# Kernel optimization log

Hardware: AMD Instinct MI355X
Metric: run time of the kernel (lower is better)

## Reference

```python
import jax, jax.numpy as jnp
import numpy as np

B, V, S, E, K, FF = 16, 512, 1024, 8, 2, 2048  # batch, n_vars, seq_len, n_experts, top_k, ff_dim


def setup_inputs() -> dict:
    key = jax.random.key(0)
    ks = jax.random.split(key, 6)
    def w(k, shape, fan_in):
        return (jax.random.normal(k, shape, jnp.float32) / np.sqrt(fan_in)).astype(jnp.float32)
    return {
        "x": jax.random.normal(ks[0], (B, S, V), jnp.float32),
        "gate_W": w(ks[1], (E, S), S),          # Gating: Linear(seq_len -> n_experts), no bias
        "exp_W": w(ks[2], (E, S, S), S),        # per-expert Linear(seq_len -> seq_len) weights
        "exp_b": jnp.zeros((E, S), jnp.float32),
        "fc1_W": w(ks[3], (FF, V), V),          # MLPFeat fc1: Linear(n_vars -> ff_dim)
        "fc1_b": jnp.zeros((FF,), jnp.float32),
        "fc2_W": w(ks[4], (V, FF), FF),         # MLPFeat fc2: Linear(ff_dim -> n_vars)
        "fc2_b": jnp.zeros((V,), jnp.float32),
    }


def reference(x, gate_W, exp_W, exp_b, fc1_W, fc1_b, fc2_W, fc2_b):
    # Dropout layers are identity at inference.
    res = x                                   # [B,S,V]
    xt = jnp.swapaxes(x, 1, 2)                # [B,V,S] tokens of dim seq_len

    # --- MLPTime (multi_expert MoE) ---
    logits = jnp.einsum('bvs,es->bve', xt, gate_W)      # [B,V,E]
    probs = jax.nn.softmax(logits, axis=-1)             # gate_logits returned by torch code
    w, sel = jax.lax.top_k(probs, K)                    # [B,V,K]
    # combine top-k weights into a dense per-expert weight [B,V,E] (zeros off top-k)
    full_w = jnp.sum(jax.nn.one_hot(sel, E, dtype=xt.dtype) * w[..., None], axis=2)
    # all-expert outputs, then weighted combine (same math as the per-expert scatter loop)
    all_out = jnp.einsum('bvs,eos->bveo', xt, exp_W) + exp_b[None, None]  # [B,V,E,S]
    moe = jnp.einsum('bve,bveo->bvo', full_w, all_out)                    # [B,V,S]
    t = jax.nn.relu(moe)

    x = jnp.swapaxes(t, 1, 2) + res           # [B,S,V] residual

    # --- MLPFeat ---
    res2 = x
    h = jax.nn.relu(x @ fc1_W.T + fc1_b)      # [B,S,FF]
    x = h @ fc2_W.T + fc2_b + res2            # [B,S,V]
    return (x, probs)
```

## Files before the change

### kernel.cpp

```cpp
#include <hip/hip_runtime.h>
#include <stdint.h>

#define B_  16
#define V_  512
#define S_  1024
#define E_  8
#define FF_ 2048
#define NT_ (B_*V_)
#define NR_ (B_*S_)

typedef __attribute__((ext_vector_type(8))) short bf16x8;
typedef __attribute__((ext_vector_type(4))) float f32x4;

__device__ __forceinline__ unsigned short f2bf(float f) {
    unsigned int u = __float_as_uint(f);
    u += 0x7FFFu + ((u >> 16) & 1u);
    return (unsigned short)(u >> 16);
}
__device__ __forceinline__ float bf2f(unsigned short u) {
    return __uint_as_float(((unsigned int)u) << 16);
}

__device__ __forceinline__ void gl_lds16(const void* g, void* l) {
    __builtin_amdgcn_global_load_lds((const __attribute__((address_space(1))) void*)g,
                                     (__attribute__((address_space(3))) void*)l,
                                     16, 0, 0);
}

__device__ __forceinline__ void cvt4(const float* s, unsigned short* d, int i) {
    float4 v = *(const float4*)(s + i);
    ushort4 o; o.x = f2bf(v.x); o.y = f2bf(v.y); o.z = f2bf(v.z); o.w = f2bf(v.w);
    *(ushort4*)(d + i) = o;
}
__global__ void k_convert3(const float* __restrict__ s0, unsigned short* __restrict__ d0, int g0,
                           const float* __restrict__ s1, unsigned short* __restrict__ d1, int g1,
                           const float* __restrict__ s2, unsigned short* __restrict__ d2) {
    int g = blockIdx.x * 256 + threadIdx.x;
    if (g < g0)           cvt4(s0, d0, g * 4);
    else if (g < g0 + g1) cvt4(s1, d1, (g - g0) * 4);
    else                  cvt4(s2, d2, (g - g0 - g1) * 4);
}

__global__ __launch_bounds__(256) void k_xt_gate(const float* __restrict__ x,
                                                 const float* __restrict__ gate_W,
                                                 unsigned short* __restrict__ xt,
                                                 double* __restrict__ part,
                                                 int* __restrict__ cnt) {
    __shared__ float t[32][33];
    __shared__ float gw[E_][128];
    int b = blockIdx.z, sc = blockIdx.y, vt = blockIdx.x;
    int tid = threadIdx.x;
    if (vt == 0 && sc == 0 && b == 0 && tid < E_) cnt[tid] = 0;
    int col = tid & 31, row8 = tid >> 5;
    for (int i = tid; i < E_ * 128; i += 256) {
        int e = i >> 7, j = i & 127;
        gw[e][j] = gate_W[e * S_ + sc * 128 + j];
    }
    double acc = 0.0;
    for (int sub = 0; sub < 4; ++sub) {
        int s0 = sc * 128 + sub * 32;
        __syncthreads();
        for (int r = 0; r < 4; ++r) {
            int sl = row8 + r * 8;
            t[sl][col] = x[(b * S_ + s0 + sl) * V_ + vt * 32 + col];
        }
        __syncthreads();
        for (int r = 0; r < 4; ++r) {
            int vl = row8 + r * 8;
            xt[(size_t)(b * V_ + vt * 32 + vl) * S_ + s0 + col] = f2bf(t[col][vl]);
        }
        #pragma unroll
        for (int s = 0; s < 32; ++s)
            acc += (double)t[s][col] * (double)gw[row8][sub * 32 + s];
    }
    int tok = b * V_ + vt * 32 + col;
    part[((size_t)sc * NT_ + tok) * E_ + row8] = acc;
}

__global__ __launch_bounds__(256) void k_gate_fin(const double* __restrict__ part,
                                                  float* __restrict__ probs_out,
                                                  int* __restrict__ cnt, int* __restrict__ tok_of,
                                                  int* __restrict__ tk_slot, float* __restrict__ tk_w) {
    int t = blockIdx.x * 256 + threadIdx.x;
    int lane = threadIdx.x & 63;
    double l[E_];
    #pragma unroll
    for (int e = 0; e < E_; ++e) l[e] = 0.0;
    for (int c = 0; c < S_ / 128; ++c) {
        const double* p = part + ((size_t)c * NT_ + t) * E_;
        #pragma unroll
        for (int e = 0; e < E_; ++e) l[e] += p[e];
    }
    double m = l[0];
    #pragma unroll
    for (int e = 1; e < E_; ++e) m = l[e] > m ? l[e] : m;
    double p[E_], sum = 0.0;
    #pragma unroll
    for (int e = 0; e < E_; ++e) { p[e] = exp(l[e] - m); sum += p[e]; }
    float pf[E_];
    #pragma unroll
    for (int e = 0; e < E_; ++e) pf[e] = (float)(p[e] / sum);
    float4 pa = {pf[0], pf[1], pf[2], pf[3]}, pb = {pf[4], pf[5], pf[6], pf[7]};
    *(float4*)(probs_out + (size_t)t * E_) = pa;
    *(float4*)(probs_out + (size_t)t * E_ + 4) = pb;
    int i0 = 0;
    #pragma unroll
    for (int e = 1; e < E_; ++e) if (pf[e] > pf[i0]) i0 = e;
    int i1 = -1;
    #pragma unroll
    for (int e = 0; e < E_; ++e) if (e != i0 && (i1 < 0 || pf[e] > pf[i1])) i1 = e;
    int sel[2] = {i0, i1};
    float wsel[2] = {pf[i0], pf[i1]};
    #pragma unroll
    for (int k = 0; k < 2; ++k) {
        int ie = sel[k];
        int pos = 0;
        for (int e = 0; e < E_; ++e) {
            unsigned long long msk = __ballot(ie == e);
            if (ie == e) {
                int rank = __popcll(msk & ((1ull << lane) - 1ull));
                int leader = __ffsll((long long)msk) - 1;
                int base = 0;
                if (lane == leader) base = atomicAdd(&cnt[e], __popcll(msk));
                base = __shfl(base, leader);
                pos = base + rank;
            }
        }
        tok_of[ie * NT_ + pos] = t;
        tk_slot[t * 2 + k] = (ie << 16) | pos;
        tk_w[t * 2 + k] = wsel[k];
    }
}

__device__ __forceinline__ void gemm_k_loop64(const unsigned short* (&ap)[4],
                                              const unsigned short* (&bp)[4],
                                              short* As, short* Bs, int kIters, int wave, int lane,
                                              f32x4 (&acc)[4][4]) {
    char* ldsA = (char*)As + wave * 4096;
    char* ldsB = (char*)Bs + wave * 4096;
    int wm = (wave & 1) << 6, wn = (wave >> 1) << 6;
    int lr = lane & 15, quad = lane >> 4;
    int pb = (quad ^ (lr & 7)) * 8;
    const unsigned short* a0 = ap[0]; const unsigned short* a1 = ap[1];
    const unsigned short* a2 = ap[2]; const unsigned short* a3 = ap[3];
    const unsigned short* b0 = bp[0]; const unsigned short* b1 = bp[1];
    const unsigned short* b2 = bp[2]; const unsigned short* b3 = bp[3];
    for (int kk = 0; kk < kIters; ++kk) {
        gl_lds16(a0, ldsA);        gl_lds16(a1, ldsA + 1024);
        gl_lds16(a2, ldsA + 2048); gl_lds16(a3, ldsA + 3072);
        gl_lds16(b0, ldsB);        gl_lds16(b1, ldsB + 1024);
        gl_lds16(b2, ldsB + 2048); gl_lds16(b3, ldsB + 3072);
        a0 += 64; a1 += 64; a2 += 64; a3 += 64;
        b0 += 64; b1 += 64; b2 += 64; b3 += 64;
        __syncthreads();
        #pragma unroll
        for (int ks = 0; ks < 2; ++ks) {
            int po = pb ^ (ks << 5);
            bf16x8 af[4], bfv[4];
            #pragma unroll
            for (int i = 0; i < 4; ++i)
                af[i] = *(const bf16x8*)(As + (wm + i * 16 + lr) * 64 + po);
            #pragma unroll
            for (int j = 0; j < 4; ++j)
                bfv[j] = *(const bf16x8*)(Bs + (wn + j * 16 + lr) * 64 + po);
            #pragma unroll
            for (int i = 0; i < 4; ++i)
                #pragma unroll
                for (int j = 0; j < 4; ++j)
                    acc[i][j] = __builtin_amdgcn_mfma_f32_16x16x32_bf16(af[i], bfv[j], acc[i][j], 0, 0, 0);
        }
        __syncthreads();
    }
}

__global__ __launch_bounds__(256, 3) void k_moe_gemm(const unsigned short* __restrict__ xt,
                                                     const unsigned short* __restrict__ expWb,
                                                     const float* __restrict__ exp_b,
                                                     const int* __restrict__ cnt,
                                                     const int* __restrict__ tok_of,
                                                     unsigned short* __restrict__ Yb) {
    int bx = ((int)(blockIdx.x & 7)) * 17 + (int)(blockIdx.x >> 3);
    int e = -1, pos0 = 0, yrow0 = 0, ne = 0;
    {
        int tb = 0, o = 0;
        #pragma unroll
        for (int i = 0; i < E_; ++i) {
            int ci = cnt[i];
            int nti = (ci + 127) >> 7;
            if (e < 0 && bx < tb + nti) { e = i; pos0 = (bx - tb) * 128; yrow0 = o; ne = ci; }
            tb += nti; o += ci;
        }
    }
    if (e < 0) return;
    int nt = blockIdx.y;
    __shared__ __align__(16) short As[128 * 64];
    __shared__ __align__(16) short Bs[128 * 64];
    int tid = threadIdx.x, wave = tid >> 6, lane = tid & 63;
    int rowLoc = wave * 32 + (lane >> 3);
    int cg = ((lane & 7) ^ ((lane >> 3) & 7)) * 8;
    const unsigned short* Wb = expWb + (size_t)e * S_ * S_;
    const unsigned short* ap[4];
    const unsigned short* bp[4];
    #pragma unroll
    for (int c = 0; c < 4; ++c) {
        int rr = rowLoc + c * 8;
        int tok = tok_of[e * NT_ + min(pos0 + rr, ne - 1)];
        ap[c] = xt + (size_t)tok * S_ + cg;
        bp[c] = Wb + (size_t)(nt * 128 + rr) * S_ + cg;
    }
    f32x4 acc[4][4] = {};
    gemm_k_loop64(ap, bp, As, Bs, S_ / 64, wave, lane, acc);
    int wm = (wave & 1) << 6, wn = (wave >> 1) << 6;
    int lr = lane & 15, quad = lane >> 4;
    #pragma unroll
    for (int i = 0; i < 4; ++i)
        #pragma unroll
        for (int r = 0; r < 4; ++r) {
            int pos = pos0 + wm + i * 16 + quad * 4 + r;
            if (pos < ne) {
                size_t row = (size_t)(yrow0 + pos);
                #pragma unroll
                for (int j = 0; j < 4; ++j) {
                    int col = nt * 128 + wn + j * 16 + lr;
                    Yb[row * S_ + col] = f2bf(acc[i][j][r] + exp_b[e * S_ + col]);
                }
            }
        }
}

__global__ void k_combine(const float* __restrict__ x, const unsigned short* __restrict__ Yb,
                          const int* __restrict__ cnt, const int* __restrict__ tk_slot,
                          const float* __restrict__ tk_w,
                          unsigned short* __restrict__ x2b) {
    __shared__ float t[32][33];
    int b = blockIdx.z, st = blockIdx.y, vt = blockIdx.x;
    int tid = threadIdx.x;
    int vl = tid >> 3, sq = (tid & 7) * 4;
    int tok = b * V_ + vt * 32 + vl;
    int s0 = tk_slot[tok * 2 + 0], s1 = tk_slot[tok * 2 + 1];
    float w0 = tk_w[tok * 2 + 0], w1 = tk_w[tok * 2 + 1];
    int e0 = s0 >> 16, e1 = s1 >> 16;
    int r0b = 0, r1b = 0, o = 0;
    #pragma unroll
    for (int i = 0; i < E_; ++i) {
        if (i == e0) r0b = o;
        if (i == e1) r1b = o;
        o += cnt[i];
    }
    size_t r0 = (size_t)(r0b + (s0 & 0xFFFF));
    size_t r1 = (size_t)(r1b + (s1 & 0xFFFF));
    int sg = st * 32 + sq;
    ushort4 y0 = *(const ushort4*)(Yb + r0 * S_ + sg);
    ushort4 y1 = *(const ushort4*)(Yb + r1 * S_ + sg);
    t[vl][sq + 0] = fmaxf(w0 * bf2f(y0.x) + w1 * bf2f(y1.x), 0.f);
    t[vl][sq + 1] = fmaxf(w0 * bf2f(y0.y) + w1 * bf2f(y1.y), 0.f);
    t[vl][sq + 2] = fmaxf(w0 * bf2f(y0.z) + w1 * bf2f(y1.z), 0.f);
    t[vl][sq + 3] = fmaxf(w0 * bf2f(y0.w) + w1 * bf2f(y1.w), 0.f);
    __syncthreads();
    int vcol = tid & 31, srow8 = tid >> 5;
    for (int r = 0; r < 4; ++r) {
        int sl = srow8 + r * 8;
        size_t gi = (size_t)(b * S_ + st * 32 + sl) * V_ + vt * 32 + vcol;
        x2b[gi] = f2bf(x[gi] + t[vcol][sl]);
    }
}

__global__ __launch_bounds__(256, 3) void k_fc1(const unsigned short* __restrict__ x2b,
                                                const unsigned short* __restrict__ w1b,
                                                const float* __restrict__ fc1_b,
                                                unsigned short* __restrict__ h) {
    __shared__ __align__(16) short As[128 * 64];
    __shared__ __align__(16) short Bs[128 * 64];
    int tid = threadIdx.x, wave = tid >> 6, lane = tid & 63;
    int rowLoc = wave * 32 + (lane >> 3);
    int cg = ((lane & 7) ^ ((lane >> 3) & 7)) * 8;
    int m0 = blockIdx.x * 128, n0 = blockIdx.y * 128;
    const unsigned short* ap[4];
    const unsigned short* bp[4];
    #pragma unroll
    for (int c = 0; c < 4; ++c) {
        int rr = rowLoc + c * 8;
        ap[c] = x2b + (size_t)(m0 + rr) * V_ + cg;
        bp[c] = w1b + (size_t)(n0 + rr) * V_ + cg;
    }
    f32x4 acc[4][4] = {};
    gemm_k_loop64(ap, bp, As, Bs, V_ / 64, wave, lane, acc);
    int wm = (wave & 1) << 6, wn = (wave >> 1) << 6;
    int lr = lane & 15, quad = lane >> 4;
    #pragma unroll
    for (int i = 0; i < 4; ++i)
        #pragma unroll
        for (int r = 0; r < 4; ++r) {
            size_t row = (size_t)(m0 + wm + i * 16 + quad * 4 + r);
            #pragma unroll
            for (int j = 0; j < 4; ++j) {
                int col = n0 + wn + j * 16 + lr;
                h[row * FF_ + col] = f2bf(fmaxf(acc[i][j][r] + fc1_b[col], 0.f));
            }
        }
}

__global__ __launch_bounds__(256, 3) void k_fc2(const unsigned short* __restrict__ h,
                                                const unsigned short* __restrict__ w2b,
                                                const float* __restrict__ fc2_b,
                                                const unsigned short* __restrict__ x2b,
                                                float* __restrict__ out) {
    __shared__ __align__(16) short As[128 * 64];
    __shared__ __align__(16) short Bs[128 * 64];
    int tid = threadIdx.x, wave = tid >> 6, lane = tid & 63;
    int rowLoc = wave * 32 + (lane >> 3);
    int cg = ((lane & 7) ^ ((lane >> 3) & 7)) * 8;
    int m0 = blockIdx.x * 128, n0 = blockIdx.y * 128;
    const unsigned short* ap[4];
    const unsigned short* bp[4];
    #pragma unroll
    for (int c = 0; c < 4; ++c) {
        int rr = rowLoc + c * 8;
        ap[c] = h + (size_t)(m0 + rr) * FF_ + cg;
        bp[c] = w2b + (size_t)(n0 + rr) * FF_ + cg;
    }
    f32x4 acc[4][4] = {};
    gemm_k_loop64(ap, bp, As, Bs, FF_ / 64, wave, lane, acc);
    int wm = (wave & 1) << 6, wn = (wave >> 1) << 6;
    int lr = lane & 15, quad = lane >> 4;
    #pragma unroll
    for (int i = 0; i < 4; ++i)
        #pragma unroll
        for (int r = 0; r < 4; ++r) {
            size_t row = (size_t)(m0 + wm + i * 16 + quad * 4 + r);
            #pragma unroll
            for (int j = 0; j < 4; ++j) {
                int col = n0 + wn + j * 16 + lr;
                out[row * V_ + col] = acc[i][j][r] + fc2_b[col] + bf2f(x2b[row * V_ + col]);
            }
        }
}

extern "C" void kernel_launch(void* const* d_in, const int* in_sizes, int n_in,
                              void* d_out, int out_size, void* d_ws, size_t ws_size,
                              hipStream_t stream) {
    const float* x      = (const float*)d_in[0];
    const float* gate_W = (const float*)d_in[1];
    const float* exp_W  = (const float*)d_in[2];
    const float* exp_b  = (const float*)d_in[3];
    const float* fc1_W  = (const float*)d_in[4];
    const float* fc1_b  = (const float*)d_in[5];
    const float* fc2_W  = (const float*)d_in[6];
    const float* fc2_b  = (const float*)d_in[7];
    float* out_x = (float*)d_out;
    float* out_p = (float*)d_out + (size_t)B_ * S_ * V_;

    if (ws_size < (size_t)155582592) return;

    char* ws = (char*)d_ws;
    unsigned short* Yb    = (unsigned short*)(ws);
    unsigned short* xt    = (unsigned short*)(ws +  67108864);
    unsigned short* x2b   = (unsigned short*)(ws + 117440512);
    unsigned short* expWb = (unsigned short*)(ws + 134217728);
    unsigned short* fc1Wb = (unsigned short*)(ws + 150994944);
    unsigned short* fc2Wb = (unsigned short*)(ws + 153092096);
    char* route = ws + 155189248;
    int*   cnt     = (int*)(route);
    int*   tok_of  = (int*)(route + 128);
    int*   tk_slot = (int*)(route + 128 + 262144);
    float* tk_w    = (float*)(route + 128 + 262144 + 65536);
    unsigned short* h = (unsigned short*)ws;
    double* part = (double*)ws;

    k_convert3<<<dim3((2097152 + 262144 + 262144) / 256), 256, 0, stream>>>(
        exp_W, expWb, 2097152, fc1_W, fc1Wb, 262144, fc2_W, fc2Wb);
    k_xt_gate<<<dim3(V_ / 32, S_ / 128, B_), 256, 0, stream>>>(x, gate_W, xt, part, cnt);
    k_gate_fin<<<dim3(NT_ / 256), 256, 0, stream>>>(part, out_p, cnt, tok_of, tk_slot, tk_w);
    k_moe_gemm<<<dim3(136, S_ / 128), 256, 0, stream>>>(xt, expWb, exp_b, cnt, tok_of, Yb);
    k_combine<<<dim3(V_ / 32, S_ / 32, B_), 256, 0, stream>>>(x, Yb, cnt, tk_slot, tk_w, x2b);
    k_fc1<<<dim3(NR_ / 128, FF_ / 128), 256, 0, stream>>>(x2b, fc1Wb, fc1_b, h);
    k_fc2<<<dim3(NR_ / 128, V_ / 128), 256, 0, stream>>>(h, fc2Wb, fc2_b, x2b, out_x);
}
```

Measured before the change: 305.7 us.

## Use 256x256 double-buffered 8-wave GEMM tiles for MoE and fc1

Replaces the 128x128 single-buffer 4-wave GEMMs for the expert projection and fc1 with a 256x256-tile, 512-thread kernel. It double-buffers LDS (128KB dynamic shared memory), prefetches the next K-slab while the current one computes, and interleaves barriers with MFMA priority hints in the ping-pong style. The aim is more data reuse per tile and overlap of global loads with MFMA work. The cost is one block per CU, larger padding waste for MoE tiles of 256 tokens, and fewer blocks for fc1. It also depends on the dynamic LDS size being accepted by the launch.

Result: slower. 330.8 us (+8.2%).

```diff
diff --git a/kernel.cpp b/kernel.cpp
--- a/kernel.cpp
+++ b/kernel.cpp
@@ -130,6 +130,170 @@
         tk_slot[t * 2 + k] = (ie << 16) | pos;
         tk_w[t * 2 + k] = wsel[k];
     }
+}
+
+__device__ __forceinline__ void stage8(const unsigned short* (&ap)[4],
+                                       const unsigned short* (&bp)[4],
+                                       char* ldsA, char* ldsB, int kt, int wave) {
+    const int off = kt * 64;
+    char* la = ldsA + wave * 4096;
+    char* lb = ldsB + wave * 4096;
+    gl_lds16(ap[0] + off, la);
+    gl_lds16(ap[1] + off, la + 1024);
+    gl_lds16(ap[2] + off, la + 2048);
+    gl_lds16(ap[3] + off, la + 3072);
+    gl_lds16(bp[0] + off, lb);
+    gl_lds16(bp[1] + off, lb + 1024);
+    gl_lds16(bp[2] + off, lb + 2048);
+    gl_lds16(bp[3] + off, lb + 3072);
+}
+
+template<bool LAST>
+__device__ __forceinline__ void body64(const short* As, const short* Bs,
+                                       int wmBase, int wnBase, int lr, int pb,
+                                       f32x4 (&acc)[8][4]) {
+    if (LAST) asm volatile("s_waitcnt vmcnt(0)" ::: "memory");
+    else      asm volatile("s_waitcnt vmcnt(8)" ::: "memory");
+    __builtin_amdgcn_s_barrier();
+    __builtin_amdgcn_sched_barrier(0);
+    bf16x8 bfv[4][2];
+    #pragma unroll
+    for (int j = 0; j < 4; ++j)
+        #pragma unroll
+        for (int ks = 0; ks < 2; ++ks)
+            bfv[j][ks] = *(const bf16x8*)(Bs + (wnBase + j * 16 + lr) * 64 + (pb ^ (ks << 5)));
+    #pragma unroll
+    for (int q = 0; q < 4; ++q) {
+        bf16x8 af[2][2];
+        #pragma unroll
+        for (int f = 0; f < 2; ++f)
+            #pragma unroll
+            for (int ks = 0; ks < 2; ++ks)
+                af[f][ks] = *(const bf16x8*)(As + (wmBase + q * 32 + f * 16 + lr) * 64 + (pb ^ (ks << 5)));
+        __builtin_amdgcn_s_barrier();
+        __builtin_amdgcn_s_setprio(1);
+        #pragma unroll
+        for (int f = 0; f < 2; ++f)
+            #pragma unroll
+            for (int j = 0; j < 4; ++j)
+                #pragma unroll
+                for (int ks = 0; ks < 2; ++ks)
+                    acc[q * 2 + f][j] = __builtin_amdgcn_mfma_f32_16x16x32_bf16(
+                        af[f][ks], bfv[j][ks], acc[q * 2 + f][j], 0, 0, 0);
+        __builtin_amdgcn_s_setprio(0);
+        __builtin_amdgcn_s_barrier();
+    }
+}
+
+template<int KT>
+__device__ __forceinline__ void gemm8(const unsigned short* (&ap)[4],
+                                      const unsigned short* (&bp)[4],
+                                      char* smem, int wave, int lane,
+                                      f32x4 (&acc)[8][4]) {
+    char* A0 = smem;           char* B0 = smem + 32768;
+    char* A1 = smem + 65536;   char* B1 = smem + 98304;
+    const int wmBase = (wave >> 2) * 128;
+    const int wnBase = (wave & 3) * 64;
+    const int lr = lane & 15;
+    const int pb = ((lane >> 4) ^ (lr & 7)) * 8;
+    stage8(ap, bp, A0, B0, 0, wave);
+    stage8(ap, bp, A1, B1, 1, wave);
+    for (int kt = 0; kt + 2 < KT; kt += 2) {
+        body64<false>((const short*)A0, (const short*)B0, wmBase, wnBase, lr, pb, acc);
+        stage8(ap, bp, A0, B0, kt + 2, wave);
+        body64<false>((const short*)A1, (const short*)B1, wmBase, wnBase, lr, pb, acc);
+        stage8(ap, bp, A1, B1, kt + 3, wave);
+    }
+    body64<false>((const short*)A0, (const short*)B0, wmBase, wnBase, lr, pb, acc);
+    body64<true >((const short*)A1, (const short*)B1, wmBase, wnBase, lr, pb, acc);
+}
+
+__global__ __launch_bounds__(512, 1) void k_moe_gemm8(const unsigned short* __restrict__ xt,
+                                                      const unsigned short* __restrict__ expWb,
+                                                      const float* __restrict__ exp_b,
+                                                      const int* __restrict__ cnt,
+                                                      const int* __restrict__ tok_of,
+                                                      unsigned short* __restrict__ Yb) {
+    int bx = ((int)(blockIdx.x & 7)) * 9 + (int)(blockIdx.x >> 3);
+    int e = -1, pos0 = 0, yrow0 = 0, ne = 0;
+    {
+        int tb = 0, o = 0;
+        #pragma unroll
+        for (int i = 0; i < E_; ++i) {
+            int ci = cnt[i];
+            int nti = (ci + 255) >> 8;
+            if (e < 0 && bx < tb + nti) { e = i; pos0 = (bx - tb) * 256; yrow0 = o; ne = ci; }
+            tb += nti; o += ci;
+        }
+    }
+    if (e < 0) return;
+    int nt = blockIdx.y;
+    extern __shared__ char smem[];
+    int tid = threadIdx.x, wave = tid >> 6, lane = tid & 63;
+    int rowLoc = wave * 32 + (lane >> 3);
+    int cg = ((lane & 7) ^ ((lane >> 3) & 7)) * 8;
+    const unsigned short* Wb = expWb + (size_t)e * S_ * S_;
+    const unsigned short* ap[4];
+    const unsigned short* bp[4];
+    #pragma unroll
+    for (int c = 0; c < 4; ++c) {
+        int rr = rowLoc + c * 8;
+        int tok = tok_of[e * NT_ + min(pos0 + rr, ne - 1)];
+        ap[c] = xt + (size_t)tok * S_ + cg;
+        bp[c] = Wb + (size_t)(nt * 256 + rr) * S_ + cg;
+    }
+    f32x4 acc[8][4] = {};
+    gemm8<S_ / 64>(ap, bp, smem, wave, lane, acc);
+    int wmBase = (wave >> 2) * 128, wnBase = (wave & 3) * 64;
+    int lr = lane & 15, quad = lane >> 4;
+    #pragma unroll
+    for (int i = 0; i < 8; ++i)
+        #pragma unroll
+        for (int r = 0; r < 4; ++r) {
+            int pos = pos0 + wmBase + i * 16 + quad * 4 + r;
+            if (pos < ne) {
+                size_t row = (size_t)(yrow0 + pos);
+                #pragma unroll
+                for (int j = 0; j < 4; ++j) {
+                    int col = nt * 256 + wnBase + j * 16 + lr;
+                    Yb[row * S_ + col] = f2bf(acc[i][j][r] + exp_b[e * S_ + col]);
+                }
+            }
+        }
+}
+
+__global__ __launch_bounds__(512, 1) void k_fc1_8p(const unsigned short* __restrict__ x2b,
+                                                   const unsigned short* __restrict__ w1b,
+                                                   const float* __restrict__ fc1_b,
+                                                   unsigned short* __restrict__ h) {
+    extern __shared__ char smem[];
+    int tid = threadIdx.x, wave = tid >> 6, lane = tid & 63;
+    int m0 = blockIdx.x * 256, n0 = blockIdx.y * 256;
+    int rowLoc = wave * 32 + (lane >> 3);
+    int cg = ((lane & 7) ^ ((lane >> 3) & 7)) * 8;
+    const unsigned short* ap[4];
+    const unsigned short* bp[4];
+    #pragma unroll
+    for (int c = 0; c < 4; ++c) {
+        int rr = rowLoc + c * 8;
+        ap[c] = x2b + (size_t)(m0 + rr) * V_ + cg;
+        bp[c] = w1b + (size_t)(n0 + rr) * V_ + cg;
+    }
+    f32x4 acc[8][4] = {};
+    gemm8<V_ / 64>(ap, bp, smem, wave, lane, acc);
+    int wmBase = (wave >> 2) * 128, wnBase = (wave & 3) * 64;
+    int lr = lane & 15, quad = lane >> 4;
+    #pragma unroll
+    for (int i = 0; i < 8; ++i)
+        #pragma unroll
+        for (int r = 0; r < 4; ++r) {
+            size_t row = (size_t)(m0 + wmBase + i * 16 + quad * 4 + r);
+            #pragma unroll
+            for (int j = 0; j < 4; ++j) {
+                int col = n0 + wnBase + j * 16 + lr;
+                h[row * FF_ + col] = f2bf(fmaxf(acc[i][j][r] + fc1_b[col], 0.f));
+            }
+        }
 }
 
 __device__ __forceinline__ void gemm_k_loop64(const unsigned short* (&ap)[4],
@@ -173,61 +337,6 @@
     }
 }
 
-__global__ __launch_bounds__(256, 3) void k_moe_gemm(const unsigned short* __restrict__ xt,
-                                                     const unsigned short* __restrict__ expWb,
-                                                     const float* __restrict__ exp_b,
-                                                     const int* __restrict__ cnt,
-                                                     const int* __restrict__ tok_of,
-                                                     unsigned short* __restrict__ Yb) {
-    int bx = ((int)(blockIdx.x & 7)) * 17 + (int)(blockIdx.x >> 3);
-    int e = -1, pos0 = 0, yrow0 = 0, ne = 0;
-    {
-        int tb = 0, o = 0;
-        #pragma unroll
-        for (int i = 0; i < E_; ++i) {
-            int ci = cnt[i];
-            int nti = (ci + 127) >> 7;
-            if (e < 0 && bx < tb + nti) { e = i; pos0 = (bx - tb) * 128; yrow0 = o; ne = ci; }
-            tb += nti; o += ci;
-        }
-    }
-    if (e < 0) return;
-    int nt = blockIdx.y;
-    __shared__ __align__(16) short As[128 * 64];
-    __shared__ __align__(16) short Bs[128 * 64];
-    int tid = threadIdx.x, wave = tid >> 6, lane = tid & 63;
-    int rowLoc = wave * 32 + (lane >> 3);
-    int cg = ((lane & 7) ^ ((lane >> 3) & 7)) * 8;
-    const unsigned short* Wb = expWb + (size_t)e * S_ * S_;
-    const unsigned short* ap[4];
-    const unsigned short* bp[4];
-    #pragma unroll
-    for (int c = 0; c < 4; ++c) {
-        int rr = rowLoc + c * 8;
-        int tok = tok_of[e * NT_ + min(pos0 + rr, ne - 1)];
-        ap[c] = xt + (size_t)tok * S_ + cg;
-        bp[c] = Wb + (size_t)(nt * 128 + rr) * S_ + cg;
-    }
-    f32x4 acc[4][4] = {};
-    gemm_k_loop64(ap, bp, As, Bs, S_ / 64, wave, lane, acc);
-    int wm = (wave & 1) << 6, wn = (wave >> 1) << 6;
-    int lr = lane & 15, quad = lane >> 4;
-    #pragma unroll
-    for (int i = 0; i < 4; ++i)
-        #pragma unroll
-        for (int r = 0; r < 4; ++r) {
-            int pos = pos0 + wm + i * 16 + quad * 4 + r;
-            if (pos < ne) {
-                size_t row = (size_t)(yrow0 + pos);
-                #pragma unroll
-                for (int j = 0; j < 4; ++j) {
-                    int col = nt * 128 + wn + j * 16 + lr;
-                    Yb[row * S_ + col] = f2bf(acc[i][j][r] + exp_b[e * S_ + col]);
-                }
-            }
-        }
-}
-
 __global__ void k_combine(const float* __restrict__ x, const unsigned short* __restrict__ Yb,
                           const int* __restrict__ cnt, const int* __restrict__ tk_slot,
                           const float* __restrict__ tk_w,
@@ -265,41 +374,6 @@
     }
 }
 
-__global__ __launch_bounds__(256, 3) void k_fc1(const unsigned short* __restrict__ x2b,
-                                                const unsigned short* __restrict__ w1b,
-                                                const float* __restrict__ fc1_b,
-                                                unsigned short* __restrict__ h) {
-    __shared__ __align__(16) short As[128 * 64];
-    __shared__ __align__(16) short Bs[128 * 64];
-    int tid = threadIdx.x, wave = tid >> 6, lane = tid & 63;
-    int rowLoc = wave * 32 + (lane >> 3);
-    int cg = ((lane & 7) ^ ((lane >> 3) & 7)) * 8;
-    int m0 = blockIdx.x * 128, n0 = blockIdx.y * 128;
-    const unsigned short* ap[4];
-    const unsigned short* bp[4];
-    #pragma unroll
-    for (int c = 0; c < 4; ++c) {
-        int rr = rowLoc + c * 8;
-        ap[c] = x2b + (size_t)(m0 + rr) * V_ + cg;
-        bp[c] = w1b + (size_t)(n0 + rr) * V_ + cg;
-    }
-    f32x4 acc[4][4] = {};
-    gemm_k_loop64(ap, bp, As, Bs, V_ / 64, wave, lane, acc);
-    int wm = (wave & 1) << 6, wn = (wave >> 1) << 6;
-    int lr = lane & 15, quad = lane >> 4;
-    #pragma unroll
-    for (int i = 0; i < 4; ++i)
-        #pragma unroll
-        for (int r = 0; r < 4; ++r) {
-            size_t row = (size_t)(m0 + wm + i * 16 + quad * 4 + r);
-            #pragma unroll
-            for (int j = 0; j < 4; ++j) {
-                int col = n0 + wn + j * 16 + lr;
-                h[row * FF_ + col] = f2bf(fmaxf(acc[i][j][r] + fc1_b[col], 0.f));
-            }
-        }
-}
-
 __global__ __launch_bounds__(256, 3) void k_fc2(const unsigned short* __restrict__ h,
                                                 const unsigned short* __restrict__ w2b,
                                                 const float* __restrict__ fc2_b,
@@ -371,8 +445,8 @@
         exp_W, expWb, 2097152, fc1_W, fc1Wb, 262144, fc2_W, fc2Wb);
     k_xt_gate<<<dim3(V_ / 32, S_ / 128, B_), 256, 0, stream>>>(x, gate_W, xt, part, cnt);
     k_gate_fin<<<dim3(NT_ / 256), 256, 0, stream>>>(part, out_p, cnt, tok_of, tk_slot, tk_w);
-    k_moe_gemm<<<dim3(136, S_ / 128), 256, 0, stream>>>(xt, expWb, exp_b, cnt, tok_of, Yb);
+    k_moe_gemm8<<<dim3(72, S_ / 256), 512, 131072, stream>>>(xt, expWb, exp_b, cnt, tok_of, Yb);
     k_combine<<<dim3(V_ / 32, S_ / 32, B_), 256, 0, stream>>>(x, Yb, cnt, tk_slot, tk_w, x2b);
-    k_fc1<<<dim3(NR_ / 128, FF_ / 128), 256, 0, stream>>>(x2b, fc1Wb, fc1_b, h);
+    k_fc1_8p<<<dim3(NR_ / 256, FF_ / 256), 512, 131072, stream>>>(x2b, fc1Wb, fc1_b, h);
     k_fc2<<<dim3(NR_ / 128, V_ / 128), 256, 0, stream>>>(h, fc2Wb, fc2_b, x2b, out_x);
 }
```
